# Optimization experiments

Hardware: AMD Instinct MI355X
Metric: run time of the kernel (lower is better)

The kernel has to match this reference:

```python
import jax, jax.numpy as jnp
import numpy as np

LAMBDA_SOFTMAX = 9.0
LAMBDA_LSE = 6.0
MARGIN = 0.2
EPS = 1e-8
NEG = -1e9


def setup_inputs() -> dict:
    key = jax.random.key(0)
    k1, k2, k3 = jax.random.split(key, 3)
    B, R, L, D = 128, 36, 48, 1024
    images = jax.random.normal(k1, (B, R, D), dtype=jnp.float32)
    captions = jax.random.normal(k2, (B, L, D), dtype=jnp.float32)
    cap_lens = jax.random.randint(k3, (B,), L // 2, L + 1, dtype=jnp.int32)
    # zero out padded words (original slices captions[:, :n_word], so padding never enters)
    wmask = (jnp.arange(L)[None, :] < cap_lens[:, None]).astype(jnp.float32)
    captions = captions * wmask[:, :, None]
    return {"images": images, "captions": captions, "cap_lens": cap_lens}


def _safe_norm_sq(q):
    # sqrt with guarded input so padded (all-zero) rows don't produce inf grads
    return jnp.sqrt(jnp.clip(q, 1e-16, None))


def _l2norm(x, axis):
    # matches l2norm: x / (sqrt(sum x^2) + eps)
    return x / (jnp.sqrt(jnp.sum(x * x, axis=axis, keepdims=True)) + EPS)


def _focal_renorm(attn, sourceL):
    # focal_equal: keep entries whose prob exceeds the row mean, then renormalize
    s = jnp.sum(attn, axis=-1, keepdims=True)
    fattn = (attn * sourceL - s > 0).astype(attn.dtype)
    tmp = fattn * attn
    ts = jnp.sum(tmp, axis=-1, keepdims=True)
    return tmp / jnp.where(ts > 0, ts, 1.0)


def reference(images, captions, cap_lens):
    C, L, D = captions.shape
    I, R, _ = images.shape
    wmask = (jnp.arange(L)[None, :] < cap_lens[:, None]).astype(captions.dtype)  # [C,L]
    caps = captions * wmask[:, :, None]
    nw = cap_lens.astype(captions.dtype)  # ragged sourceL for i2t focal

    # shared raw dot products: [C, I, L, R]
    dots = jnp.einsum('cld,ird->cilr', caps, images)

    # Gram matrices to get |weightedContext| without materializing [.,.,.,D] tensors
    img_gram = jnp.einsum('ird,isd->irs', images, images)   # [I,R,R]
    cap_gram = jnp.einsum('cld,cmd->clm', caps, caps)       # [C,L,L]
    cap_norm = _safe_norm_sq(jnp.sum(caps * caps, -1))      # [C,L]
    img_norm = _safe_norm_sq(jnp.sum(images * images, -1))  # [I,R]

    # ---------- t2i: query = caption words, context = image regions ----------
    a = jax.nn.leaky_relu(dots, 0.1)                 # raw attn (context x query^T), [C,I,L,R]
    a = _l2norm(a, axis=2)                           # l2norm over query words (dim=2 in [b,sourceL,queryL])
    a = jax.nn.softmax(a * LAMBDA_SOFTMAX, axis=-1)  # softmax over regions
    re_t = _focal_renorm(a, float(R))                # [C,I,L,R]
    # cosine(cap_word, weightedContext): w12 = sum_r re*dots; |wctx|^2 via image Gram
    w12 = jnp.sum(re_t * dots, axis=-1)                                   # [C,I,L]
    w2 = _safe_norm_sq(jnp.einsum('cilr,cils,irs->cil', re_t, re_t, img_gram))
    t2i_sim = w12 / jnp.clip(cap_norm[:, None, :] * w2, EPS, None)        # [C,I,L]
    # LogSumExp aggregation over valid words only
    t2i = jnp.log(jnp.sum(wmask[:, None, :] * jnp.exp(LAMBDA_LSE * t2i_sim), -1)) / LAMBDA_LSE  # [C,I]

    # ---------- i2t: query = image regions, context = caption words ----------
    b = jax.nn.leaky_relu(dots, 0.1)
    b = _l2norm(b, axis=3)                           # l2norm over regions (dim=2 in [b,L,R])
    logits = jnp.where(wmask[:, None, :, None] > 0, b * LAMBDA_SOFTMAX, NEG)
    b = jax.nn.softmax(logits, axis=2)               # softmax over valid words
    # focal over words, axis=2; sourceL = actual caption length (ragged)
    s = jnp.sum(b, axis=2, keepdims=True)
    fattn = (b * nw[:, None, None, None] - s > 0).astype(b.dtype)
    tmp = fattn * b
    ts = jnp.sum(tmp, axis=2, keepdims=True)
    re_i = tmp / jnp.where(ts > 0, ts, 1.0)          # [C,I,L,R]
    w12i = jnp.sum(re_i * dots, axis=2)                                   # [C,I,R]
    w2i = _safe_norm_sq(jnp.einsum('cilr,cimr,clm->cir', re_i, re_i, cap_gram))
    i2t_sim = w12i / jnp.clip(img_norm[None, :, :] * w2i, EPS, None)      # [C,I,R]
    i2t = jnp.log(jnp.sum(jnp.exp(LAMBDA_LSE * i2t_sim), -1)) / LAMBDA_LSE  # [C,I]

    scores = (t2i + i2t).T  # [n_image, n_caption]

    # ---------- margin-based ranking loss (max_violation) ----------
    d = jnp.diagonal(scores)
    cost_s = jnp.clip(MARGIN + scores - d[:, None], 0.0, None)
    cost_im = jnp.clip(MARGIN + scores - d[None, :], 0.0, None)
    eye = jnp.eye(scores.shape[0], dtype=bool)
    cost_s = jnp.where(eye, 0.0, cost_s)
    cost_im = jnp.where(eye, 0.0, cost_im)
    loss = jnp.sum(jnp.max(cost_s, axis=1)) + jnp.sum(jnp.max(cost_im, axis=0))
    return loss
```

## Files before the change

### kernel.cpp

```cpp
#include <hip/hip_runtime.h>
#include <math.h>

#define CN 128
#define INN 128
#define LN 48
#define RN 36
#define DN 1024
#define RTA 36
#define MT 6144
#define NT 4608
#define EPSF 1e-8f
#define LSM 9.0f
#define LLSE 6.0f
#define LOG2E 1.4426950408889634f

__device__ __forceinline__ float leaky(float x){ return x > 0.f ? x : 0.1f*x; }
__device__ __forceinline__ float dot4(float4 a, float4 b){
  return a.x*b.x + a.y*b.y + a.z*b.z + a.w*b.w;
}

typedef const __attribute__((address_space(1))) unsigned int* gp_t;
typedef __attribute__((address_space(3))) unsigned int* lp_t;
__device__ __forceinline__ void gload16u(const ushort* g, ushort* l) {
  __builtin_amdgcn_global_load_lds((gp_t)g, (lp_t)l, 16, 0, 0);
}

typedef short s16x8 __attribute__((ext_vector_type(8)));
typedef float f32x4 __attribute__((ext_vector_type(4)));

__device__ __forceinline__ ushort bf16rne(float f) {
  const unsigned u = __float_as_uint(f);
  return (ushort)((u + 0x7fffu + ((u>>16)&1u)) >> 16);
}
__device__ __forceinline__ float bf2f(ushort u) {
  return __uint_as_float((unsigned)u << 16);
}
__device__ __forceinline__ int swzi(int row, int col) {
  return (col & 7) | ((((col >> 3) ^ (row & 7)) & 7) << 3);
}

__global__ __launch_bounds__(256) void gram_conv_kernel(
    const float* __restrict__ imgs, const float* __restrict__ caps,
    float* __restrict__ gI, float* __restrict__ nI,
    float* __restrict__ gC, float* __restrict__ nC,
    ushort* __restrict__ aHi, ushort* __restrict__ bHi,
    ushort* __restrict__ gIb, ushort* __restrict__ gCb)
{
  __shared__ __align__(16) float L[LN*132];
  const int b = blockIdx.x, tid = threadIdx.x;
  if (b < INN) {
    const float* base = imgs + (size_t)b*RN*DN;
    const int rg = tid/12, cg = tid - (tid/12)*12;
    const bool active = tid < 216;
    float a[2][3];
    #pragma unroll
    for (int u = 0; u < 2; ++u)
      #pragma unroll
      for (int v = 0; v < 3; ++v) a[u][v] = 0.f;
    for (int d0 = 0; d0 < DN; d0 += 128) {
      __syncthreads();
      for (int idx = tid; idx < RN*32; idx += 256) {
        const int row = idx >> 5, ch = idx & 31;
        const float4 v = *(const float4*)(base + row*DN + d0 + ch*4);
        *(float4*)&L[row*132 + ch*4] = v;
        const size_t off = (size_t)(b*RN + row)*DN + d0 + ch*4;
        *(ushort4*)(bHi + off) = make_ushort4(
            bf16rne(v.x), bf16rne(v.y), bf16rne(v.z), bf16rne(v.w));
      }
      __syncthreads();
      if (active) {
        const float* r0 = &L[(2*rg)*132],   * r1 = &L[(2*rg+1)*132];
        const float* c0 = &L[(3*cg)*132],   * c1 = &L[(3*cg+1)*132], * c2 = &L[(3*cg+2)*132];
        #pragma unroll
        for (int k = 0; k < 32; ++k) {
          const float4 x0 = *(const float4*)(r0 + k*4);
          const float4 x1 = *(const float4*)(r1 + k*4);
          const float4 y0 = *(const float4*)(c0 + k*4);
          const float4 y1 = *(const float4*)(c1 + k*4);
          const float4 y2 = *(const float4*)(c2 + k*4);
          a[0][0] += dot4(x0,y0); a[0][1] += dot4(x0,y1); a[0][2] += dot4(x0,y2);
          a[1][0] += dot4(x1,y0); a[1][1] += dot4(x1,y1); a[1][2] += dot4(x1,y2);
        }
      }
    }
    if (active) {
      float* gb = gI + (size_t)b*RN*RN;
      #pragma unroll
      for (int u = 0; u < 2; ++u)
        #pragma unroll
        for (int v = 0; v < 3; ++v) {
          const int r = 2*rg + u, s = 3*cg + v;
          gb[r*RN + s] = a[u][v];
          if (r == s) nI[b*RN + r] = sqrtf(fmaxf(a[u][v], 1e-16f));
        }
    }
    __threadfence_block();
    __syncthreads();
    const float* gsrc = gI + (size_t)b*RN*RN;
    ushort* gdst = gIb + (size_t)b*3072;
    for (int idx = tid; idx < 3072; idx += 256) {
      const int row = idx >> 6, col = idx & 63;
      gdst[idx] = (row < RN && col < RN) ? bf16rne(gsrc[row*RN + col]) : (ushort)0;
    }
  } else {
    const int c = b - INN;
    const float* base = caps + (size_t)c*LN*DN;
    const int rg = tid >> 4, cg = tid & 15;
    float a[3][3];
    #pragma unroll
    for (int u = 0; u < 3; ++u)
      #pragma unroll
      for (int v = 0; v < 3; ++v) a[u][v] = 0.f;
    for (int d0 = 0; d0 < DN; d0 += 128) {
      __syncthreads();
      for (int idx = tid; idx < LN*32; idx += 256) {
        const int row = idx >> 5, ch = idx & 31;
        const float4 v = *(const float4*)(base + row*DN + d0 + ch*4);
        *(float4*)&L[row*132 + ch*4] = v;
        const size_t off = (size_t)(c*LN + row)*DN + d0 + ch*4;
        *(ushort4*)(aHi + off) = make_ushort4(
            bf16rne(v.x), bf16rne(v.y), bf16rne(v.z), bf16rne(v.w));
      }
      __syncthreads();
      const float* r0 = &L[(3*rg)*132],   * r1 = &L[(3*rg+1)*132], * r2 = &L[(3*rg+2)*132];
      const float* c0 = &L[(3*cg)*132],   * c1 = &L[(3*cg+1)*132], * c2 = &L[(3*cg+2)*132];
      #pragma unroll
      for (int k = 0; k < 32; ++k) {
        const float4 x0 = *(const float4*)(r0 + k*4);
        const float4 x1 = *(const float4*)(r1 + k*4);
        const float4 x2 = *(const float4*)(r2 + k*4);
        const float4 y0 = *(const float4*)(c0 + k*4);
        const float4 y1 = *(const float4*)(c1 + k*4);
        const float4 y2 = *(const float4*)(c2 + k*4);
        a[0][0] += dot4(x0,y0); a[0][1] += dot4(x0,y1); a[0][2] += dot4(x0,y2);
        a[1][0] += dot4(x1,y0); a[1][1] += dot4(x1,y1); a[1][2] += dot4(x1,y2);
        a[2][0] += dot4(x2,y0); a[2][1] += dot4(x2,y1); a[2][2] += dot4(x2,y2);
      }
    }
    float* gb = gC + (size_t)c*LN*LN;
    #pragma unroll
    for (int u = 0; u < 3; ++u)
      #pragma unroll
      for (int v = 0; v < 3; ++v) {
        const int r = 3*rg + u, s = 3*cg + v;
        gb[r*LN + s] = a[u][v];
        if (r == s) nC[c*LN + r] = sqrtf(fmaxf(a[u][v], 1e-16f));
      }
    __threadfence_block();
    __syncthreads();
    const float* gsrc = gC + (size_t)c*LN*LN;
    ushort* gdst = gCb + (size_t)c*3072;
    for (int idx = tid; idx < 3072; idx += 256) {
      const int row = idx >> 6, col = idx & 63;
      gdst[idx] = (col < LN) ? bf16rne(gsrc[row*LN + col]) : (ushort)0;
    }
  }
}

__global__ __launch_bounds__(256) void dots_gemm_mfma(
    const ushort* __restrict__ aHi, const ushort* __restrict__ bHi,
    float* __restrict__ dots, int arow0)
{
  __shared__ __align__(16) ushort sT[16384];
  const int tid = threadIdx.x;
  const int wv = tid >> 6, lane = tid & 63;
  const int l15 = lane & 15, kg = lane >> 4;
  const int wr = wv >> 1, wc = wv & 1;
  const int M0 = blockIdx.y * 128;
  const int N0 = blockIdx.x * 128;

  int offA[4], offB[4];
  #pragma unroll
  for (int f = 0; f < 4; ++f) {
    offA[f] = (wr*64 + f*16 + l15)*64;
    offB[f] = (wc*64 + f*16 + l15)*64;
  }
  int srow[4], sgk[4]; unsigned dOff[4];
  #pragma unroll
  for (int h = 0; h < 4; ++h) {
    const int ch = h*256 + tid;
    const int row = ch >> 3, gp = ch & 7;
    srow[h] = row;
    sgk[h] = (gp ^ (row & 7)) * 8;
    dOff[h] = (unsigned)(h*256 + wv*64) * 8;
  }

  f32x4 acc[4][4];
  #pragma unroll
  for (int mf = 0; mf < 4; ++mf)
    #pragma unroll
    for (int nf = 0; nf < 4; ++nf) acc[mf][nf] = (f32x4){0.f,0.f,0.f,0.f};

  const size_t aR = (size_t)(arow0 + M0);
  for (int k0 = 0; k0 < DN; k0 += 64) {
    __syncthreads();
    #pragma unroll
    for (int h = 0; h < 4; ++h) {
      const size_t ao = (aR + srow[h])*DN + k0 + sgk[h];
      const size_t bo = ((size_t)(N0 + srow[h]))*DN + k0 + sgk[h];
      gload16u(aHi + ao, sT + dOff[h]);
      gload16u(bHi + bo, sT + 8192 + dOff[h]);
    }
    asm volatile("s_waitcnt vmcnt(0)" ::: "memory");
    __syncthreads();
    #pragma unroll
    for (int ks = 0; ks < 2; ++ks) {
      s16x8 ah[4], bh[4];
      #pragma unroll
      for (int f = 0; f < 4; ++f) {
        const int rA = wr*64 + f*16 + l15;
        const int rB = wc*64 + f*16 + l15;
        ah[f] = *(const s16x8*)&sT[offA[f] + (((ks*4+kg) ^ (rA&7)))*8];
        bh[f] = *(const s16x8*)&sT[8192 + offB[f] + (((ks*4+kg) ^ (rB&7)))*8];
      }
      #pragma unroll
      for (int mf = 0; mf < 4; ++mf)
        #pragma unroll
        for (int nf = 0; nf < 4; ++nf)
          acc[mf][nf] = __builtin_amdgcn_mfma_f32_16x16x32_bf16(ah[mf], bh[nf], acc[mf][nf], 0,0,0);
    }
  }
  #pragma unroll
  for (int mf = 0; mf < 4; ++mf)
    #pragma unroll
    for (int nf = 0; nf < 4; ++nf) {
      const int n = N0 + wc*64 + nf*16 + l15;
      #pragma unroll
      for (int r = 0; r < 4; ++r) {
        const int m = M0 + wr*64 + mf*16 + kg*4 + r;
        dots[(size_t)m*NT + n] = acc[mf][nf][r];
      }
    }
}

__global__ __launch_bounds__(256) void attn_kernel(
    const float* __restrict__ dots, const int* __restrict__ cap_lens,
    const ushort* __restrict__ gIb, const ushort* __restrict__ gCb,
    const float* __restrict__ nI, const float* __restrict__ nC,
    float* __restrict__ scores, int cbase)
{
  __shared__ float sDots[LN][RTA+1];
  __shared__ __align__(16) ushort sMeT[LN*64];
  __shared__ __align__(16) ushort sMeIT[48*64];
  __shared__ float sQqT[LN], sQqI[48];
  __shared__ float sW12t[LN], sInvT[LN];
  __shared__ float sW12i[RN], sInvI[RN];
  __shared__ float sColInv[RN], sRowInv[LN];
  __shared__ float sCapN[LN], sImgN[RN];
  __shared__ float sEt[LN], sEi[RN];
  __shared__ float sRed[2];

  const int cl = blockIdx.y;
  const int c  = cbase + cl;
  const int it = blockIdx.x;
  const int tid = threadIdx.x;
  const int lane = tid & 63, wv = tid >> 6;
  const int l15 = lane & 15, kg = lane >> 4;
  const int team = tid >> 2, q4 = tid & 3;
  const int nw = cap_lens[c];
  const float nwf = (float)nw;

  for (int idx = tid; idx < LN*RTA/4; idx += 256) {
    const int l = idx / (RTA/4), jseg = idx - l*(RTA/4);
    const float4 v = *(const float4*)(dots + ((size_t)cl*LN + l)*NT + (size_t)it*RTA + jseg*4);
    float* dst = &sDots[l][jseg*4];
    dst[0]=v.x; dst[1]=v.y; dst[2]=v.z; dst[3]=v.w;
  }
  for (int idx = tid; idx < 768; idx += 256) {
    if (idx < 384) ((uint4*)sMeT)[idx] = make_uint4(0,0,0,0);
    else ((uint4*)sMeIT)[idx-384] = make_uint4(0,0,0,0);
  }
  if (tid < LN) { sCapN[tid] = nC[c*LN + tid]; sQqT[tid] = 0.f; }
  if (tid >= 64 && tid < 64+48) sQqI[tid-64] = 0.f;
  if (tid >= 128 && tid < 128+RN) sImgN[tid-128] = nI[it*RN + (tid-128)];
  __syncthreads();

  #pragma unroll 1
  for (int pass = 0; pass < 2; ++pass) {
    const int vrow = pass*64 + team;
    if (vrow < RN) {
      float s = 0.f;
      #pragma unroll
      for (int j = 0; j < 12; ++j) { const float v = leaky(sDots[q4*12+j][vrow]); s += v*v; }
      s += __shfl_xor(s, 1, 4); s += __shfl_xor(s, 2, 4);
      if (q4 == 0) sColInv[vrow] = (LSM*LOG2E) * __builtin_amdgcn_rcpf(sqrtf(s) + EPSF);
    } else if (vrow < RN + LN) {
      const int l = vrow - RN;
      float s = 0.f;
      #pragma unroll
      for (int j = 0; j < 9; ++j) { const float v = leaky(sDots[l][q4*9+j]); s += v*v; }
      s += __shfl_xor(s, 1, 4); s += __shfl_xor(s, 2, 4);
      if (q4 == 0) sRowInv[l] = (LSM*LOG2E) * __builtin_amdgcn_rcpf(sqrtf(s) + EPSF);
    }
  }
  __syncthreads();

  #pragma unroll 1
  for (int pass = 0; pass < 2; ++pass) {
    const int vrow = pass*64 + team;
    if (vrow < LN) {
      const int l = vrow;
      const int cb = q4*9;
      float d9[9], x9[9];
      #pragma unroll
      for (int j = 0; j < 9; ++j) d9[j] = sDots[l][cb + j];
      float se = 0.f;
      #pragma unroll
      for (int j = 0; j < 9; ++j) {
        const float e = exp2f(leaky(d9[j]) * sColInv[cb + j]);
        x9[j] = e; se += e;
      }
      se += __shfl_xor(se, 1, 4); se += __shfl_xor(se, 2, 4);
      float ts = 0.f;
      #pragma unroll
      for (int j = 0; j < 9; ++j) {
        const float me = (x9[j]*36.f > se) ? x9[j] : 0.f;
        x9[j] = me; ts += me;
      }
      ts += __shfl_xor(ts, 1, 4); ts += __shfl_xor(ts, 2, 4);
      float w12 = 0.f;
      #pragma unroll
      for (int j = 0; j < 9; ++j) w12 += x9[j]*d9[j];
      w12 += __shfl_xor(w12, 1, 4); w12 += __shfl_xor(w12, 2, 4);
      #pragma unroll
      for (int j = 0; j < 9; ++j)
        sMeT[l*64 + swzi(l, cb + j)] = bf16rne(x9[j]);
      if (q4 == 0) {
        sW12t[l] = w12;
        sInvT[l] = __builtin_amdgcn_rcpf((ts > 0.f) ? ts : 1.f);
      }
    } else {
      const int r = vrow - LN;
      if (r < RN) {
        float d12[12], x12[12];
        #pragma unroll
        for (int j = 0; j < 12; ++j) d12[j] = sDots[q4*12+j][r];
        float se = 0.f;
        #pragma unroll
        for (int j = 0; j < 12; ++j) {
          const int l = q4*12 + j;
          const float e = (l < nw) ? exp2f(leaky(d12[j]) * sRowInv[l]) : 0.f;
          x12[j] = e; se += e;
        }
        se += __shfl_xor(se, 1, 4); se += __shfl_xor(se, 2, 4);
        float ts = 0.f;
        #pragma unroll
        for (int j = 0; j < 12; ++j) {
          const float me = (x12[j]*nwf > se) ? x12[j] : 0.f;
          x12[j] = me; ts += me;
        }
        ts += __shfl_xor(ts, 1, 4); ts += __shfl_xor(ts, 2, 4);
        float w12 = 0.f;
        #pragma unroll
        for (int j = 0; j < 12; ++j) w12 += x12[j]*d12[j];
        w12 += __shfl_xor(w12, 1, 4); w12 += __shfl_xor(w12, 2, 4);
        #pragma unroll
        for (int j = 0; j < 12; ++j)
          sMeIT[r*64 + swzi(r, q4*12 + j)] = bf16rne(x12[j]);
        if (q4 == 0) {
          sW12i[r] = w12;
          sInvI[r] = __builtin_amdgcn_rcpf((ts > 0.f) ? ts : 1.f);
        }
      }
    }
  }
  __syncthreads();

  const ushort* gIbase = gIb + (size_t)it*3072;
  const ushort* gCbase = gCb + (size_t)c*3072;
  #pragma unroll 1
  for (int t = wv; t < 18; t += 4) {
    const bool isT = (t < 9);
    const int tt = isT ? t : t - 9;
    const int mt = tt / 3, nt = tt - 3*(tt/3);
    const ushort* Ab = isT ? gIbase : gCbase;
    const ushort* Mb = isT ? sMeT   : sMeIT;
    const int arow = mt*16 + l15;
    const int brow = nt*16 + l15;
    f32x4 acc = (f32x4){0.f,0.f,0.f,0.f};
    #pragma unroll
    for (int ks = 0; ks < 2; ++ks) {
      const s16x8 af = *(const s16x8*)(Ab + arow*64 + (ks*4+kg)*8);
      const s16x8 bf = *(const s16x8*)&Mb[brow*64 + (((ks*4+kg) ^ (brow&7)))*8];
      acc = __builtin_amdgcn_mfma_f32_16x16x32_bf16(af, bf, acc, 0,0,0);
    }
    float part = 0.f;
    #pragma unroll
    for (int rg = 0; rg < 4; ++rg) {
      const int orow = mt*16 + kg*4 + rg;
      part += acc[rg] * bf2f(Mb[brow*64 + swzi(brow, orow)]);
    }
    part += __shfl_xor(part, 16);
    part += __shfl_xor(part, 32);
    if (lane < 16)
      atomicAdd(isT ? &sQqT[nt*16 + l15] : &sQqI[nt*16 + l15], part);
  }
  __syncthreads();

  if (tid < LN) {
    const float invd = sInvT[tid];
    const float w2 = sqrtf(fmaxf(sQqT[tid]*invd*invd, 1e-16f));
    const float sim = (sW12t[tid]*invd) * __builtin_amdgcn_rcpf(fmaxf(sCapN[tid]*w2, EPSF));
    sEt[tid] = (tid < nw) ? exp2f((LLSE*LOG2E)*sim) : 0.f;
  }
  if (tid >= 64 && tid < 64+RN) {
    const int r = tid - 64;
    const float invd = sInvI[r];
    const float w2 = sqrtf(fmaxf(sQqI[r]*invd*invd, 1e-16f));
    const float sim = (sW12i[r]*invd) * __builtin_amdgcn_rcpf(fmaxf(sImgN[r]*w2, EPSF));
    sEi[r] = exp2f((LLSE*LOG2E)*sim);
  }
  __syncthreads();
  if (wv == 0) {
    float e = (lane < LN) ? sEt[lane] : 0.f;
    #pragma unroll
    for (int o = 32; o > 0; o >>= 1) e += __shfl_xor(e, o);
    if (lane == 0) sRed[0] = e;
  } else if (wv == 1) {
    float e = (lane < RN) ? sEi[lane] : 0.f;
    #pragma unroll
    for (int o = 32; o > 0; o >>= 1) e += __shfl_xor(e, o);
    if (lane == 0) sRed[1] = e;
  }
  __syncthreads();
  if (tid == 0)
    scores[(size_t)it*CN + c] = log2f(sRed[0]*sRed[1]) * (1.f/(LLSE*LOG2E));
}

__global__ __launch_bounds__(128) void loss_kernel(
    const float* __restrict__ S, float* __restrict__ out)
{
  __shared__ float red[128];
  const int t = threadIdx.x;
  const float d = S[t*CN + t];
  float m1 = -1e30f, m2 = -1e30f;
  for (int cc = 0; cc < CN; ++cc)
    if (cc != t) m1 = fmaxf(m1, 0.2f + S[t*CN+cc] - d);
  for (int i2 = 0; i2 < INN; ++i2)
    if (i2 != t) m2 = fmaxf(m2, 0.2f + S[i2*CN+t] - d);
  red[t] = fmaxf(m1, 0.f) + fmaxf(m2, 0.f);
  __syncthreads();
  for (int s = 64; s > 0; s >>= 1) {
    if (t < s) red[t] += red[t+s];
    __syncthreads();
  }
  if (t == 0) out[0] = red[0];
}

extern "C" void kernel_launch(void* const* d_in, const int* in_sizes, int n_in,
                              void* d_out, int out_size, void* d_ws, size_t ws_size,
                              hipStream_t stream) {
  (void)in_sizes; (void)n_in; (void)out_size;
  const float* imgs = (const float*)d_in[0];
  const float* caps = (const float*)d_in[1];
  const int*   lens = (const int*)d_in[2];

  const size_t bfUS = 2*((size_t)MT + NT)*DN;
  const size_t gbUS = (size_t)(INN + CN)*3072;
  const size_t smallF = (size_t)INN*RN*RN + INN*RN + (size_t)CN*LN*LN + CN*LN + (size_t)INN*CN;
  int g = CN;
  while (g > 8) {
    const size_t need = (bfUS + gbUS)*2 + (smallF + (size_t)g*LN*NT)*4;
    if (need <= ws_size) break;
    g >>= 1;
  }

  ushort* aHi = (ushort*)d_ws;
  ushort* aLo = aHi + (size_t)MT*DN;
  ushort* bHi = aLo + (size_t)MT*DN;
  ushort* bLo = bHi + (size_t)NT*DN;
  ushort* gIb = bLo + (size_t)NT*DN;
  ushort* gCb = gIb + (size_t)INN*3072;
  float* fbase = (float*)(gCb + (size_t)CN*3072);
  float* gI     = fbase;
  float* nI     = gI + (size_t)INN*RN*RN;
  float* gC     = nI + (size_t)INN*RN;
  float* nC     = gC + (size_t)CN*LN*LN;
  float* scores = nC + (size_t)CN*LN;
  float* dots   = scores + (size_t)INN*CN;

  gram_conv_kernel<<<dim3(INN+CN), dim3(256), 0, stream>>>(
      imgs, caps, gI, nI, gC, nC, aHi, bHi, gIb, gCb);
  for (int c0 = 0; c0 < CN; c0 += g) {
    dots_gemm_mfma<<<dim3(NT/128, g*LN/128), dim3(256), 0, stream>>>(
        aHi, bHi, dots, c0*LN);
    attn_kernel<<<dim3(INN, g), dim3(256), 0, stream>>>(
        dots, lens, gIb, gCb, nI, nC, scores, c0);
  }
  loss_kernel<<<dim3(1), dim3(128), 0, stream>>>(scores, (float*)d_out);
}
```

Baseline: 277.9 us.

## Split bf16 conversion into its own kernel and compute Gram matrices with MFMA

```diff
diff --git a/kernel.cpp b/kernel.cpp
--- a/kernel.cpp
+++ b/kernel.cpp
@@ -15,9 +15,6 @@
 #define LOG2E 1.4426950408889634f
 
 __device__ __forceinline__ float leaky(float x){ return x > 0.f ? x : 0.1f*x; }
-__device__ __forceinline__ float dot4(float4 a, float4 b){
-  return a.x*b.x + a.y*b.y + a.z*b.z + a.w*b.w;
-}
 
 typedef const __attribute__((address_space(1))) unsigned int* gp_t;
 typedef __attribute__((address_space(3))) unsigned int* lp_t;
@@ -39,121 +36,78 @@
   return (col & 7) | ((((col >> 3) ^ (row & 7)) & 7) << 3);
 }
 
-__global__ __launch_bounds__(256) void gram_conv_kernel(
-    const float* __restrict__ imgs, const float* __restrict__ caps,
-    float* __restrict__ gI, float* __restrict__ nI,
-    float* __restrict__ gC, float* __restrict__ nC,
-    ushort* __restrict__ aHi, ushort* __restrict__ bHi,
+__global__ __launch_bounds__(256) void conv_kernel(
+    const float* __restrict__ caps, const float* __restrict__ imgs,
+    ushort* __restrict__ aHi, ushort* __restrict__ bHi)
+{
+  const int NA = MT*DN/4, NB = NT*DN/4;
+  for (int i = blockIdx.x*256 + threadIdx.x; i < NA + NB; i += gridDim.x*256) {
+    const float4 v = (i < NA) ? ((const float4*)caps)[i] : ((const float4*)imgs)[i - NA];
+    const ushort4 h = make_ushort4(bf16rne(v.x), bf16rne(v.y), bf16rne(v.z), bf16rne(v.w));
+    if (i < NA) ((ushort4*)aHi)[i] = h;
+    else        ((ushort4*)bHi)[i-NA] = h;
+  }
+}
+
+__global__ __launch_bounds__(256) void gram_mfma_kernel(
+    const ushort* __restrict__ aHi, const ushort* __restrict__ bHi,
+    float* __restrict__ nI, float* __restrict__ nC,
     ushort* __restrict__ gIb, ushort* __restrict__ gCb)
 {
-  __shared__ __align__(16) float L[LN*132];
+  __shared__ __align__(16) ushort sX[48*64];
   const int b = blockIdx.x, tid = threadIdx.x;
-  if (b < INN) {
-    const float* base = imgs + (size_t)b*RN*DN;
-    const int rg = tid/12, cg = tid - (tid/12)*12;
-    const bool active = tid < 216;
-    float a[2][3];
-    #pragma unroll
-    for (int u = 0; u < 2; ++u)
-      #pragma unroll
-      for (int v = 0; v < 3; ++v) a[u][v] = 0.f;
-    for (int d0 = 0; d0 < DN; d0 += 128) {
-      __syncthreads();
-      for (int idx = tid; idx < RN*32; idx += 256) {
-        const int row = idx >> 5, ch = idx & 31;
-        const float4 v = *(const float4*)(base + row*DN + d0 + ch*4);
-        *(float4*)&L[row*132 + ch*4] = v;
-        const size_t off = (size_t)(b*RN + row)*DN + d0 + ch*4;
-        *(ushort4*)(bHi + off) = make_ushort4(
-            bf16rne(v.x), bf16rne(v.y), bf16rne(v.z), bf16rne(v.w));
-      }
-      __syncthreads();
-      if (active) {
-        const float* r0 = &L[(2*rg)*132],   * r1 = &L[(2*rg+1)*132];
-        const float* c0 = &L[(3*cg)*132],   * c1 = &L[(3*cg+1)*132], * c2 = &L[(3*cg+2)*132];
-        #pragma unroll
-        for (int k = 0; k < 32; ++k) {
-          const float4 x0 = *(const float4*)(r0 + k*4);
-          const float4 x1 = *(const float4*)(r1 + k*4);
-          const float4 y0 = *(const float4*)(c0 + k*4);
-          const float4 y1 = *(const float4*)(c1 + k*4);
-          const float4 y2 = *(const float4*)(c2 + k*4);
-          a[0][0] += dot4(x0,y0); a[0][1] += dot4(x0,y1); a[0][2] += dot4(x0,y2);
-          a[1][0] += dot4(x1,y0); a[1][1] += dot4(x1,y1); a[1][2] += dot4(x1,y2);
+  const bool isImg = b < INN;
+  const int R = isImg ? RN : LN;
+  const ushort* X = isImg ? (bHi + (size_t)b*RN*DN) : (aHi + (size_t)(b-INN)*LN*DN);
+  ushort* gOut = isImg ? (gIb + (size_t)b*3072) : (gCb + (size_t)(b-INN)*3072);
+  float* nOut = isImg ? (nI + b*RN) : (nC + (b-INN)*LN);
+  const int lane = tid & 63, wv = tid >> 6;
+  const int l15 = lane & 15, kg = lane >> 4;
+
+  f32x4 acc[3];
+  #pragma unroll
+  for (int i = 0; i < 3; ++i) acc[i] = (f32x4){0.f,0.f,0.f,0.f};
+
+  for (int k0 = 0; k0 < DN; k0 += 64) {
+    __syncthreads();
+    for (int idx = tid; idx < R*8; idx += 256) {
+      const int row = idx >> 3, gp = idx & 7;
+      *(uint4*)&sX[row*64 + (gp ^ (row&7))*8] =
+        *(const uint4*)(X + (size_t)row*DN + k0 + gp*8);
+    }
+    __syncthreads();
+    #pragma unroll
+    for (int i = 0; i < 3; ++i) {
+      const int tt = wv + 4*i;
+      if (tt < 9) {
+        const int mt = tt/3, nt = tt - 3*(tt/3);
+        #pragma unroll
+        for (int ks = 0; ks < 2; ++ks) {
+          const int rA = mt*16 + l15, rB = nt*16 + l15;
+          const s16x8 af = *(const s16x8*)&sX[rA*64 + (((ks*4+kg) ^ (rA&7)))*8];
+          const s16x8 bf = *(const s16x8*)&sX[rB*64 + (((ks*4+kg) ^ (rB&7)))*8];
+          acc[i] = __builtin_amdgcn_mfma_f32_16x16x32_bf16(af, bf, acc[i], 0,0,0);
         }
       }
     }
-    if (active) {
-      float* gb = gI + (size_t)b*RN*RN;
-      #pragma unroll
-      for (int u = 0; u < 2; ++u)
-        #pragma unroll
-        for (int v = 0; v < 3; ++v) {
-          const int r = 2*rg + u, s = 3*cg + v;
-          gb[r*RN + s] = a[u][v];
-          if (r == s) nI[b*RN + r] = sqrtf(fmaxf(a[u][v], 1e-16f));
-        }
-    }
-    __threadfence_block();
-    __syncthreads();
-    const float* gsrc = gI + (size_t)b*RN*RN;
-    ushort* gdst = gIb + (size_t)b*3072;
-    for (int idx = tid; idx < 3072; idx += 256) {
-      const int row = idx >> 6, col = idx & 63;
-      gdst[idx] = (row < RN && col < RN) ? bf16rne(gsrc[row*RN + col]) : (ushort)0;
-    }
-  } else {
-    const int c = b - INN;
-    const float* base = caps + (size_t)c*LN*DN;
-    const int rg = tid >> 4, cg = tid & 15;
-    float a[3][3];
-    #pragma unroll
-    for (int u = 0; u < 3; ++u)
-      #pragma unroll
-      for (int v = 0; v < 3; ++v) a[u][v] = 0.f;
-    for (int d0 = 0; d0 < DN; d0 += 128) {
-      __syncthreads();
-      for (int idx = tid; idx < LN*32; idx += 256) {
-        const int row = idx >> 5, ch = idx & 31;
-        const float4 v = *(const float4*)(base + row*DN + d0 + ch*4);
-        *(float4*)&L[row*132 + ch*4] = v;
-        const size_t off = (size_t)(c*LN + row)*DN + d0 + ch*4;
-        *(ushort4*)(aHi + off) = make_ushort4(
-            bf16rne(v.x), bf16rne(v.y), bf16rne(v.z), bf16rne(v.w));
-      }
-      __syncthreads();
-      const float* r0 = &L[(3*rg)*132],   * r1 = &L[(3*rg+1)*132], * r2 = &L[(3*rg+2)*132];
-      const float* c0 = &L[(3*cg)*132],   * c1 = &L[(3*cg+1)*132], * c2 = &L[(3*cg+2)*132];
-      #pragma unroll
-      for (int k = 0; k < 32; ++k) {
-        const float4 x0 = *(const float4*)(r0 + k*4);
-        const float4 x1 = *(const float4*)(r1 + k*4);
-        const float4 x2 = *(const float4*)(r2 + k*4);
-        const float4 y0 = *(const float4*)(c0 + k*4);
-        const float4 y1 = *(const float4*)(c1 + k*4);
-        const float4 y2 = *(const float4*)(c2 + k*4);
-        a[0][0] += dot4(x0,y0); a[0][1] += dot4(x0,y1); a[0][2] += dot4(x0,y2);
-        a[1][0] += dot4(x1,y0); a[1][1] += dot4(x1,y1); a[1][2] += dot4(x1,y2);
-        a[2][0] += dot4(x2,y0); a[2][1] += dot4(x2,y1); a[2][2] += dot4(x2,y2);
-      }
-    }
-    float* gb = gC + (size_t)c*LN*LN;
-    #pragma unroll
-    for (int u = 0; u < 3; ++u)
-      #pragma unroll
-      for (int v = 0; v < 3; ++v) {
-        const int r = 3*rg + u, s = 3*cg + v;
-        gb[r*LN + s] = a[u][v];
-        if (r == s) nC[c*LN + r] = sqrtf(fmaxf(a[u][v], 1e-16f));
-      }
-    __threadfence_block();
-    __syncthreads();
-    const float* gsrc = gC + (size_t)c*LN*LN;
-    ushort* gdst = gCb + (size_t)c*3072;
-    for (int idx = tid; idx < 3072; idx += 256) {
-      const int row = idx >> 6, col = idx & 63;
-      gdst[idx] = (col < LN) ? bf16rne(gsrc[row*LN + col]) : (ushort)0;
-    }
+  }
+  #pragma unroll
+  for (int i = 0; i < 3; ++i) {
+    const int tt = wv + 4*i;
+    if (tt < 9) {
+      const int mt = tt/3, nt = tt - 3*(tt/3);
+      #pragma unroll
+      for (int rg = 0; rg < 4; ++rg) {
+        const int m = mt*16 + kg*4 + rg, n = nt*16 + l15;
+        const float cv = acc[i][rg];
+        gOut[m*64 + n] = (m < R && n < R) ? bf16rne(cv) : (ushort)0;
+        if (m == n && m < R) nOut[m] = sqrtf(fmaxf(cv, 1e-16f));
+      }
+    }
+  }
+  for (int idx = tid; idx < 48*16; idx += 256) {
+    const int row = idx >> 4, col = 48 + (idx & 15);
+    gOut[row*64 + col] = 0;
   }
 }
 
@@ -479,8 +433,9 @@
   float* scores = nC + (size_t)CN*LN;
   float* dots   = scores + (size_t)INN*CN;
 
-  gram_conv_kernel<<<dim3(INN+CN), dim3(256), 0, stream>>>(
-      imgs, caps, gI, nI, gC, nC, aHi, bHi, gIb, gCb);
+  conv_kernel<<<dim3(1024), dim3(256), 0, stream>>>(caps, imgs, aHi, bHi);
+  gram_mfma_kernel<<<dim3(INN+CN), dim3(256), 0, stream>>>(
+      aHi, bHi, nI, nC, gIb, gCb);
   for (int c0 = 0; c0 < CN; c0 += g) {
     dots_gemm_mfma<<<dim3(NT/128, g*LN/128), dim3(256), 0, stream>>>(
         aHi, bHi, dots, c0*LN);
```

Measured after the change: 250.2 us. -10.0%, faster.
